# Kernel optimization log

Measured on AMD Instinct MI355X. Metric: run time of the kernel, lower is better.

Reference implementation:

```python
import jax, jax.numpy as jnp
import numpy as np
import math

N_HEADS = 16
DIM = 1024
D_HEAD = DIM // N_HEADS
BS, QLEN = 2, 2048


def setup_inputs() -> dict:
    key = jax.random.key(0)
    ks = jax.random.split(key, 10)
    s = 0.02
    return {
        "input": jax.random.normal(ks[0], (BS, QLEN, DIM), dtype=jnp.float32),
        "mask": jnp.ones((BS, QLEN), dtype=jnp.int32),
        "q_w": jax.random.normal(ks[1], (DIM, DIM), dtype=jnp.float32) * s,
        "q_b": jax.random.normal(ks[2], (DIM,), dtype=jnp.float32) * s,
        "k_w": jax.random.normal(ks[3], (DIM, DIM), dtype=jnp.float32) * s,
        "k_b": jax.random.normal(ks[4], (DIM,), dtype=jnp.float32) * s,
        "v_w": jax.random.normal(ks[5], (DIM, DIM), dtype=jnp.float32) * s,
        "v_b": jax.random.normal(ks[6], (DIM,), dtype=jnp.float32) * s,
        "o_w": jax.random.normal(ks[7], (DIM, DIM), dtype=jnp.float32) * s,
        "o_b": jax.random.normal(ks[8], (DIM,), dtype=jnp.float32) * s,
    }


def _shape(x, bs):
    # (bs, len, dim) -> (bs, heads, len, d_head)
    return x.reshape(bs, -1, N_HEADS, D_HEAD).transpose(0, 2, 1, 3)


def reference(input, mask, q_w, q_b, k_w, k_b, v_w, v_b, o_w, o_b):
    bs, qlen, dim = input.shape
    # projections (torch Linear: x @ W^T + b)
    q = _shape(input @ q_w.T + q_b, bs)
    k = _shape(input @ k_w.T + k_b, bs)
    v = _shape(input @ v_w.T + v_b, bs)
    q = q / math.sqrt(D_HEAD)
    # scores: (bs, heads, qlen, klen)
    scores = jnp.einsum("bhqd,bhkd->bhqk", q, k)
    pad = (mask == 0)[:, None, None, :]  # (bs,1,1,klen)
    scores = jnp.where(pad, -jnp.inf, scores)
    weights = jax.nn.softmax(scores.astype(jnp.float32), axis=-1).astype(scores.dtype)
    # dropout p=0.0 (eval) -> identity
    context = jnp.einsum("bhqk,bhkd->bhqd", weights, v)
    context = context.transpose(0, 2, 1, 3).reshape(bs, qlen, dim)
    return context @ o_w.T + o_b
```

## Files before the change

### kernel.cpp

```cpp
#include <hip/hip_runtime.h>


#define BS    2
#define QLEN  2048
#define DIM   1024
#define NH    16
#define DH    64
#define MTOK  (BS * QLEN)

#define QSCALE 0.18033688011112042f

typedef __attribute__((ext_vector_type(8))) short short8;
typedef __attribute__((ext_vector_type(4))) float float4_t;
typedef __attribute__((ext_vector_type(4))) int   int4_t;

__device__ __forceinline__ ushort f2bf(float f) {
    unsigned u = __float_as_uint(f);
    return (ushort)((u + 0x7fffu + ((u >> 16) & 1u)) >> 16);
}
__device__ __forceinline__ short8 pack8(float4 a0, float4 a1) {
    short8 r;
    r[0] = (short)f2bf(a0.x); r[1] = (short)f2bf(a0.y);
    r[2] = (short)f2bf(a0.z); r[3] = (short)f2bf(a0.w);
    r[4] = (short)f2bf(a1.x); r[5] = (short)f2bf(a1.y);
    r[6] = (short)f2bf(a1.z); r[7] = (short)f2bf(a1.w);
    return r;
}

__device__ __forceinline__ void glds16(const void* g, void* l) {
    __builtin_amdgcn_global_load_lds(
        (const __attribute__((address_space(1))) unsigned int*)g,
        (__attribute__((address_space(3))) unsigned int*)l, 16, 0, 0);
}

__global__ __launch_bounds__(256) void conv_all(
    const float* __restrict__ x,  const float* __restrict__ qw,
    const float* __restrict__ kw, const float* __restrict__ vw,
    const float* __restrict__ ow,
    ushort* __restrict__ Xbf, ushort* __restrict__ Wbf)
{
    const int blk = blockIdx.x;
    const float* s; ushort* d; size_t base;
    if (blk < 4096)      { s = x;  d = Xbf;             base = (size_t)blk * 1024; }
    else if (blk < 5120) { s = qw; d = Wbf;             base = (size_t)(blk - 4096) * 1024; }
    else if (blk < 6144) { s = kw; d = Wbf + 1048576;   base = (size_t)(blk - 5120) * 1024; }
    else if (blk < 7168) { s = vw; d = Wbf + 2097152;   base = (size_t)(blk - 6144) * 1024; }
    else                 { s = ow; d = Wbf + 3145728;   base = (size_t)(blk - 7168) * 1024; }
    const size_t i = base + threadIdx.x * 4;
    float4 v = *(const float4*)(s + i);
    ushort4 o;
    o.x = f2bf(v.x); o.y = f2bf(v.y); o.z = f2bf(v.z); o.w = f2bf(v.w);
    *(ushort4*)(d + i) = o;
}

__global__ __launch_bounds__(256) void transpose_v(
    const ushort* __restrict__ Vrow, ushort* __restrict__ Vt)
{
    __shared__ ushort T[64][72];
    const int tid  = threadIdx.x;
    const int tile = blockIdx.x;
    const int bh   = blockIdx.y;
    const int b = bh >> 4, h = bh & 15;

    #pragma unroll
    for (int rep = 0; rep < 2; ++rep) {
        int ch = tid + rep * 256;
        int tok = ch >> 3, seg = ch & 7;
        uint4 v = *(const uint4*)(Vrow + (size_t)(b * QLEN + tile * 64 + tok) * DIM
                                        + h * DH + seg * 8);
        *(uint4*)&T[tok][seg * 8] = v;
    }
    __syncthreads();
    #pragma unroll
    for (int rep = 0; rep < 2; ++rep) {
        int ch = tid + rep * 256;
        int dim = ch >> 3, tseg = ch & 7;
        ushort t0 = T[tseg * 8 + 0][dim], t1 = T[tseg * 8 + 1][dim];
        ushort t2 = T[tseg * 8 + 2][dim], t3 = T[tseg * 8 + 3][dim];
        ushort t4 = T[tseg * 8 + 4][dim], t5 = T[tseg * 8 + 5][dim];
        ushort t6 = T[tseg * 8 + 6][dim], t7 = T[tseg * 8 + 7][dim];
        uint4 o;
        o.x = (unsigned)t0 | ((unsigned)t1 << 16);
        o.y = (unsigned)t2 | ((unsigned)t3 << 16);
        o.z = (unsigned)t4 | ((unsigned)t5 << 16);
        o.w = (unsigned)t6 | ((unsigned)t7 << 16);
        *(uint4*)(Vt + (size_t)bh * DH * QLEN + (size_t)dim * QLEN
                      + tile * 64 + tseg * 8) = o;
    }
}

__global__ __launch_bounds__(256) void gemm_qkv(
    const ushort* __restrict__ A, const ushort* __restrict__ Bw,
    const float* __restrict__ bias0, const float* __restrict__ bias1,
    const float* __restrict__ bias2,
    ushort* __restrict__ outQ, ushort* __restrict__ outK, ushort* __restrict__ outVt)
{
    __shared__ ushort As[128 * 32];
    __shared__ ushort Bs[128 * 32];
    const int tid  = threadIdx.x;
    const int w    = tid >> 6;
    const int lane = tid & 63;
    const int r15  = lane & 15;
    const int quad = lane >> 4;
    const int nblk = 3072 >> 7;
    const int brow = blockIdx.x / nblk;
    const int bcol = blockIdx.x - brow * nblk;
    const int wrow = (w >> 1) * 64;
    const int wcol = (w & 1) * 64;
    const int K = DIM;

    float4_t acc[4][4];
    #pragma unroll
    for (int i = 0; i < 4; ++i)
        #pragma unroll
        for (int j = 0; j < 4; ++j)
            acc[i][j] = (float4_t){0.f, 0.f, 0.f, 0.f};

    int ch0 = w * 64 + lane;
    int ch1 = ch0 + 256;
    const int row0 = ch0 >> 2, s0 = ch0 & 3, gk0 = s0 ^ ((row0 >> 1) & 3);
    const int row1 = ch1 >> 2, s1 = ch1 & 3, gk1 = s1 ^ ((row1 >> 1) & 3);

    const ushort* ga0 = A + (size_t)(brow * 128 + row0) * K + gk0 * 8;
    const ushort* ga1 = A + (size_t)(brow * 128 + row1) * K + gk1 * 8;
    const ushort* gb0 = Bw + (size_t)(bcol * 128 + row0) * K + gk0 * 8;
    const ushort* gb1 = Bw + (size_t)(bcol * 128 + row1) * K + gk1 * 8;

    for (int k0 = 0; k0 < K; k0 += 32) {
        __syncthreads();
        glds16(ga0 + k0, As + ch0 * 8);
        glds16(ga1 + k0, As + ch1 * 8);
        glds16(gb0 + k0, Bs + ch0 * 8);
        glds16(gb1 + k0, Bs + ch1 * 8);
        __syncthreads();

        short8 af[4], bf[4];
        #pragma unroll
        for (int ms = 0; ms < 4; ++ms) {
            int row = wrow + ms * 16 + r15;
            int s = quad ^ ((row >> 1) & 3);
            af[ms] = *(const short8*)&As[row * 32 + s * 8];
        }
        #pragma unroll
        for (int ns = 0; ns < 4; ++ns) {
            int row = wcol + ns * 16 + r15;
            int s = quad ^ ((row >> 1) & 3);
            bf[ns] = *(const short8*)&Bs[row * 32 + s * 8];
        }
        #pragma unroll
        for (int ms = 0; ms < 4; ++ms)
            #pragma unroll
            for (int ns = 0; ns < 4; ++ns)
                acc[ms][ns] = __builtin_amdgcn_mfma_f32_16x16x32_bf16(
                    af[ms], bf[ns], acc[ms][ns], 0, 0, 0);
    }

    #pragma unroll
    for (int ms = 0; ms < 4; ++ms) {
        const int rowg = brow * 128 + wrow + ms * 16 + quad * 4;
        #pragma unroll
        for (int ns = 0; ns < 4; ++ns) {
            const int colg = bcol * 128 + wcol + ns * 16 + r15;
            if (colg < 1024) {
                const float bb = bias0[colg];
                #pragma unroll
                for (int r = 0; r < 4; ++r)
                    outQ[(size_t)(rowg + r) * 1024 + colg] =
                        f2bf((acc[ms][ns][r] + bb) * QSCALE);
            } else if (colg < 2048) {
                const float bb = bias1[colg - 1024];
                #pragma unroll
                for (int r = 0; r < 4; ++r)
                    outK[(size_t)(rowg + r) * 1024 + (colg - 1024)] =
                        f2bf(acc[ms][ns][r] + bb);
            } else {
                const int vcol = colg - 2048;
                const int hh = vcol >> 6, dd = vcol & 63;
                const float bb = bias2[vcol];
                const int bidx = rowg >> 11;
                const int tloc = rowg & 2047;
                ushort4 o4;
                o4.x = f2bf(acc[ms][ns][0] + bb);
                o4.y = f2bf(acc[ms][ns][1] + bb);
                o4.z = f2bf(acc[ms][ns][2] + bb);
                o4.w = f2bf(acc[ms][ns][3] + bb);
                *(ushort4*)&outVt[((size_t)(bidx * 16 + hh) * 64 + dd) * QLEN + tloc] = o4;
            }
        }
    }
}

__global__ __launch_bounds__(256) void gemm_o(
    const ushort* __restrict__ A, const ushort* __restrict__ Bw,
    const float* __restrict__ bias, float* __restrict__ Out)
{
    __shared__ ushort As[128 * 32];
    __shared__ ushort Bs[64 * 32];
    const int tid  = threadIdx.x;
    const int w    = tid >> 6;
    const int lane = tid & 63;
    const int r15  = lane & 15;
    const int quad = lane >> 4;
    const int brow = blockIdx.x >> 4;
    const int bcol = blockIdx.x & 15;
    const int wrow = w * 32;
    const int K = DIM;

    float4_t acc[2][4];
    #pragma unroll
    for (int i = 0; i < 2; ++i)
        #pragma unroll
        for (int j = 0; j < 4; ++j)
            acc[i][j] = (float4_t){0.f, 0.f, 0.f, 0.f};

    const int chA0 = w * 64 + lane, chA1 = chA0 + 256;
    const int rA0 = chA0 >> 2, sA0 = chA0 & 3, gkA0 = sA0 ^ ((rA0 >> 1) & 3);
    const int rA1 = chA1 >> 2, sA1 = chA1 & 3, gkA1 = sA1 ^ ((rA1 >> 1) & 3);
    const int rB  = tid >> 2,  sB  = tid & 3,  gkB  = sB  ^ ((rB  >> 1) & 3);

    const ushort* ga0 = A + (size_t)(brow * 128 + rA0) * K + gkA0 * 8;
    const ushort* ga1 = A + (size_t)(brow * 128 + rA1) * K + gkA1 * 8;
    const ushort* gb  = Bw + (size_t)(bcol * 64 + rB) * K + gkB * 8;

    for (int k0 = 0; k0 < K; k0 += 32) {
        __syncthreads();
        glds16(ga0 + k0, As + chA0 * 8);
        glds16(ga1 + k0, As + chA1 * 8);
        glds16(gb + k0,  Bs + tid * 8);
        __syncthreads();

        short8 af[2], bf[4];
        #pragma unroll
        for (int ms = 0; ms < 2; ++ms) {
            int row = wrow + ms * 16 + r15;
            int s = quad ^ ((row >> 1) & 3);
            af[ms] = *(const short8*)&As[row * 32 + s * 8];
        }
        #pragma unroll
        for (int ns = 0; ns < 4; ++ns) {
            int row = ns * 16 + r15;
            int s = quad ^ ((row >> 1) & 3);
            bf[ns] = *(const short8*)&Bs[row * 32 + s * 8];
        }
        #pragma unroll
        for (int ms = 0; ms < 2; ++ms)
            #pragma unroll
            for (int ns = 0; ns < 4; ++ns)
                acc[ms][ns] = __builtin_amdgcn_mfma_f32_16x16x32_bf16(
                    af[ms], bf[ns], acc[ms][ns], 0, 0, 0);
    }

    #pragma unroll
    for (int ms = 0; ms < 2; ++ms) {
        const int rowg = brow * 128 + wrow + ms * 16 + quad * 4;
        #pragma unroll
        for (int ns = 0; ns < 4; ++ns) {
            const int colg = bcol * 64 + ns * 16 + r15;
            const float bb = bias[colg];
            #pragma unroll
            for (int r = 0; r < 4; ++r)
                Out[(size_t)(rowg + r) * 1024 + colg] = acc[ms][ns][r] + bb;
        }
    }
}

__global__ __launch_bounds__(256) void gemm_f32in_bf16out(
    const float* __restrict__ X, const float* __restrict__ W,
    const float* __restrict__ B, ushort* __restrict__ Out,
    int M, int N, int K, float scale)
{
    const int lane = threadIdx.x & 63;
    const int wid  = (blockIdx.x * blockDim.x + threadIdx.x) >> 6;
    const int tilesN = N >> 4;
    const int tm = wid / tilesN;
    const int tn = wid - tm * tilesN;
    const int r15  = lane & 15;
    const int quad = lane >> 4;

    const float* xp = X + (size_t)(tm * 16 + r15) * K + quad * 8;
    const float* wp = W + (size_t)(tn * 16 + r15) * K + quad * 8;

    float4_t acc = {0.f, 0.f, 0.f, 0.f};
    for (int k0 = 0; k0 < K; k0 += 32) {
        float4 a0 = *(const float4*)(xp + k0);
        float4 a1 = *(const float4*)(xp + k0 + 4);
        float4 b0 = *(const float4*)(wp + k0);
        float4 b1 = *(const float4*)(wp + k0 + 4);
        acc = __builtin_amdgcn_mfma_f32_16x16x32_bf16(pack8(a0, a1), pack8(b0, b1), acc, 0, 0, 0);
    }
    const int col  = tn * 16 + r15;
    const float bias = B[col];
    const int row0 = tm * 16 + quad * 4;
    #pragma unroll
    for (int r = 0; r < 4; ++r)
        Out[(size_t)(row0 + r) * N + col] = f2bf((acc[r] + bias) * scale);
}

__global__ __launch_bounds__(256) void gemm_bf16in_f32out(
    const ushort* __restrict__ X, const float* __restrict__ W,
    const float* __restrict__ B, float* __restrict__ Out,
    int M, int N, int K)
{
    const int lane = threadIdx.x & 63;
    const int wid  = (blockIdx.x * blockDim.x + threadIdx.x) >> 6;
    const int tilesN = N >> 4;
    const int tm = wid / tilesN;
    const int tn = wid - tm * tilesN;
    const int r15  = lane & 15;
    const int quad = lane >> 4;

    const ushort* xp = X + (size_t)(tm * 16 + r15) * K + quad * 8;
    const float*  wp = W + (size_t)(tn * 16 + r15) * K + quad * 8;

    float4_t acc = {0.f, 0.f, 0.f, 0.f};
    for (int k0 = 0; k0 < K; k0 += 32) {
        short8 a = *(const short8*)(xp + k0);
        float4 b0 = *(const float4*)(wp + k0);
        float4 b1 = *(const float4*)(wp + k0 + 4);
        acc = __builtin_amdgcn_mfma_f32_16x16x32_bf16(a, pack8(b0, b1), acc, 0, 0, 0);
    }
    const int col  = tn * 16 + r15;
    const float bias = B[col];
    const int row0 = tm * 16 + quad * 4;
    #pragma unroll
    for (int r = 0; r < 4; ++r)
        Out[(size_t)(row0 + r) * N + col] = acc[r] + bias;
}

__global__ __launch_bounds__(256) void flash_attn(
    const ushort* __restrict__ Qb, const ushort* __restrict__ Kb,
    const ushort* __restrict__ Vt, const int* __restrict__ mask,
    ushort* __restrict__ Cb)
{
    __shared__ __align__(16) ushort Ks[2][64][64];
    __shared__ __align__(16) ushort Vs[2][64][64];
    __shared__ __align__(16) float  Mb[QLEN];
    __shared__ int Kflag[QLEN / 64];

    const int tid  = threadIdx.x;
    const int w    = tid >> 6;
    const int lane = tid & 63;
    const int r15  = lane & 15;
    const int quad = lane >> 4;
    const int bh = blockIdx.y;
    const int b = bh >> 4, h = bh & 15;

    {
        const int4* m4 = (const int4*)(mask + b * QLEN);
        #pragma unroll
        for (int rep = 0; rep < 2; ++rep) {
            const int idx = tid + rep * 256;
            int4 mv = m4[idx];
            float4 o;
            o.x = mv.x ? 0.f : -INFINITY;
            o.y = mv.y ? 0.f : -INFINITY;
            o.z = mv.z ? 0.f : -INFINITY;
            o.w = mv.w ? 0.f : -INFINITY;
            *(float4*)&Mb[idx * 4] = o;
        }
    }

    const int qbase = blockIdx.x * 128 + w * 32;
    const ushort* qp = Qb + (size_t)(b * QLEN + qbase + r15) * DIM + h * DH + quad * 8;
    short8 qf[2][2];
    qf[0][0] = *(const short8*)(qp);
    qf[0][1] = *(const short8*)(qp + 32);
    qf[1][0] = *(const short8*)(qp + 16 * DIM);
    qf[1][1] = *(const short8*)(qp + 16 * DIM + 32);

    const ushort* kg = Kb + (size_t)b * QLEN * DIM + h * DH;
    const ushort* vg = Vt + (size_t)bh * DH * QLEN;

    const int a0 = tid >> 3, seg = tid & 7;
    const int krow0 = (((a0 & 7) >> 2) << 4) + (((a0 >> 3) & 3) << 2) + (a0 & 3);
    const int sK = (seg ^ (krow0 & 7)) << 3;
    const int sV = (seg ^ (a0 & 7)) << 3;
    const int xq = (quad ^ (r15 & 7)) << 3;

    float4_t o[2][4];
    float4_t ol[2];
    #pragma unroll
    for (int rg = 0; rg < 2; ++rg) {
        ol[rg] = (float4_t){0.f, 0.f, 0.f, 0.f};
        #pragma unroll
        for (int ds = 0; ds < 4; ++ds)
            o[rg][ds] = (float4_t){0.f, 0.f, 0.f, 0.f};
    }
    short8 ones8;
    #pragma unroll
    for (int i = 0; i < 8; ++i) ones8[i] = (short)0x3F80;

    uint4 kr0 = *(const uint4*)(kg + (size_t)(a0     ) * DIM + seg * 8);
    uint4 kr1 = *(const uint4*)(kg + (size_t)(a0 + 32) * DIM + seg * 8);
    uint4 vr0 = *(const uint4*)(vg + (size_t)(a0     ) * QLEN + seg * 8);
    uint4 vr1 = *(const uint4*)(vg + (size_t)(a0 + 32) * QLEN + seg * 8);
    *(uint4*)&Ks[0][krow0     ][sK] = kr0;
    *(uint4*)&Ks[0][krow0 + 32][sK] = kr1;
    *(uint4*)&Vs[0][a0        ][sV] = vr0;
    *(uint4*)&Vs[0][a0 + 32   ][sV] = vr1;
    __syncthreads();

    if (tid < QLEN / 64) {
        const float4* m4 = (const float4*)&Mb[tid * 64];
        float acc = 0.f;
        #pragma unroll
        for (int i = 0; i < 16; ++i) {
            float4 v = m4[i];
            acc += v.x + v.y + v.z + v.w;
        }
        Kflag[tid] = (acc < -1e30f) ? 1 : 0;
    }
    __syncthreads();

    int p = 0;
    for (int kt = 0; kt < QLEN; kt += 64) {
        const bool more = (kt + 64 < QLEN);
        if (more) {
            kr0 = *(const uint4*)(kg + (size_t)(kt + 64 + a0     ) * DIM + seg * 8);
            kr1 = *(const uint4*)(kg + (size_t)(kt + 64 + a0 + 32) * DIM + seg * 8);
            vr0 = *(const uint4*)(vg + (size_t)(a0     ) * QLEN + kt + 64 + seg * 8);
            vr1 = *(const uint4*)(vg + (size_t)(a0 + 32) * QLEN + kt + 64 + seg * 8);
        }
        const int hasmask = Kflag[kt >> 6];

        int pk[4][2][2];
        #pragma unroll
        for (int ks = 0; ks < 4; ++ks) {
            const ushort* krow = &Ks[p][ks * 16 + r15][0];
            short8 kf0 = *(const short8*)(krow + xq);
            short8 kf1 = *(const short8*)(krow + (xq ^ 32));
            #pragma unroll
            for (int rg = 0; rg < 2; ++rg) {
                float4_t s = {0.f, 0.f, 0.f, 0.f};
                s = __builtin_amdgcn_mfma_f32_16x16x32_bf16(kf0, qf[rg][0], s, 0, 0, 0);
                s = __builtin_amdgcn_mfma_f32_16x16x32_bf16(kf1, qf[rg][1], s, 0, 0, 0);
                unsigned u0, u1, u2, u3;
                if (hasmask) {
                    const float4 mb = *(const float4*)&Mb[kt + ((ks >> 1) << 5)
                                                           + (quad << 3) + ((ks & 1) << 2)];
                    u0 = __float_as_uint(__builtin_amdgcn_exp2f(s[0] + mb.x));
                    u1 = __float_as_uint(__builtin_amdgcn_exp2f(s[1] + mb.y));
                    u2 = __float_as_uint(__builtin_amdgcn_exp2f(s[2] + mb.z));
                    u3 = __float_as_uint(__builtin_amdgcn_exp2f(s[3] + mb.w));
                } else {
                    u0 = __float_as_uint(__builtin_amdgcn_exp2f(s[0]));
                    u1 = __float_as_uint(__builtin_amdgcn_exp2f(s[1]));
                    u2 = __float_as_uint(__builtin_amdgcn_exp2f(s[2]));
                    u3 = __float_as_uint(__builtin_amdgcn_exp2f(s[3]));
                }
                pk[ks][rg][0] = __builtin_amdgcn_perm(u1, u0, 0x07060302);
                pk[ks][rg][1] = __builtin_amdgcn_perm(u3, u2, 0x07060302);
            }
        }

        #pragma unroll
        for (int ck = 0; ck < 2; ++ck) {
            short8 vf[4];
            #pragma unroll
            for (int ds = 0; ds < 4; ++ds)
                vf[ds] = *(const short8*)(&Vs[p][ds * 16 + r15][0] + (xq ^ (ck << 5)));
            #pragma unroll
            for (int rg = 0; rg < 2; ++rg) {
                int4_t pfi = { pk[2 * ck][rg][0], pk[2 * ck][rg][1],
                               pk[2 * ck + 1][rg][0], pk[2 * ck + 1][rg][1] };
                short8 pf = __builtin_bit_cast(short8, pfi);
                #pragma unroll
                for (int ds = 0; ds < 4; ++ds)
                    o[rg][ds] = __builtin_amdgcn_mfma_f32_16x16x32_bf16(
                        pf, vf[ds], o[rg][ds], 0, 0, 0);
                ol[rg] = __builtin_amdgcn_mfma_f32_16x16x32_bf16(
                    pf, ones8, ol[rg], 0, 0, 0);
            }
        }

        if (more) {
            *(uint4*)&Ks[p ^ 1][krow0     ][sK] = kr0;
            *(uint4*)&Ks[p ^ 1][krow0 + 32][sK] = kr1;
            *(uint4*)&Vs[p ^ 1][a0        ][sV] = vr0;
            *(uint4*)&Vs[p ^ 1][a0 + 32   ][sV] = vr1;
        }
        __syncthreads();
        p ^= 1;
    }

    #pragma unroll
    for (int rg = 0; rg < 2; ++rg) {
        #pragma unroll
        for (int r = 0; r < 4; ++r) {
            const float ir = 1.f / fmaxf(ol[rg][r], 1e-30f);
            const size_t rb = (size_t)(b * QLEN + qbase + rg * 16 + quad * 4 + r) * DIM
                              + h * DH;
            Cb[rb +  0 + r15] = f2bf(o[rg][0][r] * ir);
            Cb[rb + 16 + r15] = f2bf(o[rg][1][r] * ir);
            Cb[rb + 32 + r15] = f2bf(o[rg][2][r] * ir);
            Cb[rb + 48 + r15] = f2bf(o[rg][3][r] * ir);
        }
    }
}

extern "C" void kernel_launch(void* const* d_in, const int* in_sizes, int n_in,
                              void* d_out, int out_size, void* d_ws, size_t ws_size,
                              hipStream_t stream)
{
    const float* x    = (const float*)d_in[0];
    const int*   mask = (const int*)d_in[1];
    const float* q_w  = (const float*)d_in[2];
    const float* q_b  = (const float*)d_in[3];
    const float* k_w  = (const float*)d_in[4];
    const float* k_b  = (const float*)d_in[5];
    const float* v_w  = (const float*)d_in[6];
    const float* v_b  = (const float*)d_in[7];
    const float* o_w  = (const float*)d_in[8];
    const float* o_b  = (const float*)d_in[9];
    float* out = (float*)d_out;

    const size_t SEG = (size_t)MTOK * DIM;
    ushort* Qbf = (ushort*)d_out;
    ushort* Xbf = Qbf + SEG;
    ushort* Kb  = (ushort*)d_ws;
    ushort* Cb  = Kb + SEG;
    ushort* Vt  = Cb + SEG;
    ushort* Wbf = Vt + SEG;

    const bool big = ws_size >= (size_t)32 * 1024 * 1024;

    if (big) {
        conv_all<<<8192, 256, 0, stream>>>(x, q_w, k_w, v_w, o_w, Xbf, Wbf);
        gemm_qkv<<<(MTOK / 128) * (3072 / 128), 256, 0, stream>>>(
            Xbf, Wbf, q_b, k_b, v_b, Qbf, Kb, Vt);

        flash_attn<<<dim3(QLEN / 128, BS * NH), 256, 0, stream>>>(Qbf, Kb, Vt, mask, Cb);

        gemm_o<<<(MTOK / 128) * (DIM / 64), 256, 0, stream>>>(
            Cb, Wbf + 3 * (size_t)(DIM * DIM), o_b, out);
    } else {
        const int tiles   = (MTOK / 16) * (DIM / 16);
        const int gblocks = tiles / 4;
        gemm_f32in_bf16out<<<gblocks, 256, 0, stream>>>(x, q_w, q_b, Qbf, MTOK, DIM, DIM, QSCALE);
        gemm_f32in_bf16out<<<gblocks, 256, 0, stream>>>(x, k_w, k_b, Kb,  MTOK, DIM, DIM, 1.0f);
        gemm_f32in_bf16out<<<gblocks, 256, 0, stream>>>(x, v_w, v_b, Cb,  MTOK, DIM, DIM, 1.0f);
        transpose_v<<<dim3(QLEN / 64, BS * NH), 256, 0, stream>>>(Cb, Vt);
        flash_attn<<<dim3(QLEN / 128, BS * NH), 256, 0, stream>>>(Qbf, Kb, Vt, mask, Cb);
        gemm_bf16in_f32out<<<tiles / 4, 256, 0, stream>>>(Cb, o_w, o_b, out, MTOK, DIM, DIM);
    }
}
```

Before: 216.8 us.

## Double K-step in GEMMs and process two KV tiles per flash iteration

Both projection GEMMs now load a 64-wide K slice per iteration, using a new 8-way XOR swizzle, which halves the number of barrier pairs per K loop. The flash attention kernel stages two 64-key tiles at once (128 keys per iteration) instead of ping-pong double buffering, which halves the number of loop trips and barriers. It also removes the per-tile mask-flag precomputation and always adds the mask bias before exp2. The trade-off is more LDS per GEMM block, less overlap between global loads and compute in attention because a barrier now precedes the LDS writes, and extra adds where the mask is all ones.

```diff
diff --git a/kernel.cpp b/kernel.cpp
--- a/kernel.cpp
+++ b/kernel.cpp
@@ -95,8 +95,8 @@
     const float* __restrict__ bias2,
     ushort* __restrict__ outQ, ushort* __restrict__ outK, ushort* __restrict__ outVt)
 {
-    __shared__ ushort As[128 * 32];
-    __shared__ ushort Bs[128 * 32];
+    __shared__ ushort As[128 * 64];
+    __shared__ ushort Bs[128 * 64];
     const int tid  = threadIdx.x;
     const int w    = tid >> 6;
     const int lane = tid & 63;
@@ -116,43 +116,46 @@
         for (int j = 0; j < 4; ++j)
             acc[i][j] = (float4_t){0.f, 0.f, 0.f, 0.f};
 
-    int ch0 = w * 64 + lane;
-    int ch1 = ch0 + 256;
-    const int row0 = ch0 >> 2, s0 = ch0 & 3, gk0 = s0 ^ ((row0 >> 1) & 3);
-    const int row1 = ch1 >> 2, s1 = ch1 & 3, gk1 = s1 ^ ((row1 >> 1) & 3);
-
-    const ushort* ga0 = A + (size_t)(brow * 128 + row0) * K + gk0 * 8;
-    const ushort* ga1 = A + (size_t)(brow * 128 + row1) * K + gk1 * 8;
-    const ushort* gb0 = Bw + (size_t)(bcol * 128 + row0) * K + gk0 * 8;
-    const ushort* gb1 = Bw + (size_t)(bcol * 128 + row1) * K + gk1 * 8;
-
-    for (int k0 = 0; k0 < K; k0 += 32) {
+    int chS[4];
+    const ushort* gaS[4];
+    const ushort* gbS[4];
+    #pragma unroll
+    for (int rep = 0; rep < 4; ++rep) {
+        const int ch  = w * 256 + rep * 64 + lane;
+        const int row = ch >> 3;
+        const int g   = (ch & 7) ^ (row & 7);
+        chS[rep] = ch;
+        gaS[rep] = A  + (size_t)(brow * 128 + row) * K + g * 8;
+        gbS[rep] = Bw + (size_t)(bcol * 128 + row) * K + g * 8;
+    }
+    const int xg = r15 & 7;
+
+    for (int k0 = 0; k0 < K; k0 += 64) {
         __syncthreads();
-        glds16(ga0 + k0, As + ch0 * 8);
-        glds16(ga1 + k0, As + ch1 * 8);
-        glds16(gb0 + k0, Bs + ch0 * 8);
-        glds16(gb1 + k0, Bs + ch1 * 8);
+        #pragma unroll
+        for (int rep = 0; rep < 4; ++rep) {
+            glds16(gaS[rep] + k0, As + chS[rep] * 8);
+            glds16(gbS[rep] + k0, Bs + chS[rep] * 8);
+        }
         __syncthreads();
 
-        short8 af[4], bf[4];
-        #pragma unroll
-        for (int ms = 0; ms < 4; ++ms) {
-            int row = wrow + ms * 16 + r15;
-            int s = quad ^ ((row >> 1) & 3);
-            af[ms] = *(const short8*)&As[row * 32 + s * 8];
-        }
-        #pragma unroll
-        for (int ns = 0; ns < 4; ++ns) {
-            int row = wcol + ns * 16 + r15;
-            int s = quad ^ ((row >> 1) & 3);
-            bf[ns] = *(const short8*)&Bs[row * 32 + s * 8];
-        }
-        #pragma unroll
-        for (int ms = 0; ms < 4; ++ms)
+        #pragma unroll
+        for (int hh = 0; hh < 2; ++hh) {
+            const int ph = ((hh * 4 + quad) ^ xg) * 8;
+            short8 af[4], bf[4];
+            #pragma unroll
+            for (int ms = 0; ms < 4; ++ms)
+                af[ms] = *(const short8*)&As[(wrow + ms * 16 + r15) * 64 + ph];
             #pragma unroll
             for (int ns = 0; ns < 4; ++ns)
-                acc[ms][ns] = __builtin_amdgcn_mfma_f32_16x16x32_bf16(
-                    af[ms], bf[ns], acc[ms][ns], 0, 0, 0);
+                bf[ns] = *(const short8*)&Bs[(wcol + ns * 16 + r15) * 64 + ph];
+            #pragma unroll
+            for (int ms = 0; ms < 4; ++ms)
+                #pragma unroll
+                for (int ns = 0; ns < 4; ++ns)
+                    acc[ms][ns] = __builtin_amdgcn_mfma_f32_16x16x32_bf16(
+                        af[ms], bf[ns], acc[ms][ns], 0, 0, 0);
+        }
     }
 
     #pragma unroll
@@ -194,8 +197,8 @@
     const ushort* __restrict__ A, const ushort* __restrict__ Bw,
     const float* __restrict__ bias, float* __restrict__ Out)
 {
-    __shared__ ushort As[128 * 32];
-    __shared__ ushort Bs[64 * 32];
+    __shared__ ushort As[128 * 64];
+    __shared__ ushort Bs[64 * 64];
     const int tid  = threadIdx.x;
     const int w    = tid >> 6;
     const int lane = tid & 63;
@@ -213,41 +216,53 @@
         for (int j = 0; j < 4; ++j)
             acc[i][j] = (float4_t){0.f, 0.f, 0.f, 0.f};
 
-    const int chA0 = w * 64 + lane, chA1 = chA0 + 256;
-    const int rA0 = chA0 >> 2, sA0 = chA0 & 3, gkA0 = sA0 ^ ((rA0 >> 1) & 3);
-    const int rA1 = chA1 >> 2, sA1 = chA1 & 3, gkA1 = sA1 ^ ((rA1 >> 1) & 3);
-    const int rB  = tid >> 2,  sB  = tid & 3,  gkB  = sB  ^ ((rB  >> 1) & 3);
-
-    const ushort* ga0 = A + (size_t)(brow * 128 + rA0) * K + gkA0 * 8;
-    const ushort* ga1 = A + (size_t)(brow * 128 + rA1) * K + gkA1 * 8;
-    const ushort* gb  = Bw + (size_t)(bcol * 64 + rB) * K + gkB * 8;
-
-    for (int k0 = 0; k0 < K; k0 += 32) {
+    int chA[4];  const ushort* gaS[4];
+    #pragma unroll
+    for (int rep = 0; rep < 4; ++rep) {
+        const int ch  = w * 256 + rep * 64 + lane;
+        const int row = ch >> 3;
+        const int g   = (ch & 7) ^ (row & 7);
+        chA[rep] = ch;
+        gaS[rep] = A + (size_t)(brow * 128 + row) * K + g * 8;
+    }
+    int chB[2];  const ushort* gbS[2];
+    #pragma unroll
+    for (int rep = 0; rep < 2; ++rep) {
+        const int ch  = w * 128 + rep * 64 + lane;
+        const int row = ch >> 3;
+        const int g   = (ch & 7) ^ (row & 7);
+        chB[rep] = ch;
+        gbS[rep] = Bw + (size_t)(bcol * 64 + row) * K + g * 8;
+    }
+    const int xg = r15 & 7;
+
+    for (int k0 = 0; k0 < K; k0 += 64) {
         __syncthreads();
-        glds16(ga0 + k0, As + chA0 * 8);
-        glds16(ga1 + k0, As + chA1 * 8);
-        glds16(gb + k0,  Bs + tid * 8);
+        #pragma unroll
+        for (int rep = 0; rep < 4; ++rep)
+            glds16(gaS[rep] + k0, As + chA[rep] * 8);
+        #pragma unroll
+        for (int rep = 0; rep < 2; ++rep)
+            glds16(gbS[rep] + k0, Bs + chB[rep] * 8);
         __syncthreads();
 
-        short8 af[2], bf[4];
-        #pragma unroll
-        for (int ms = 0; ms < 2; ++ms) {
-            int row = wrow + ms * 16 + r15;
-            int s = quad ^ ((row >> 1) & 3);
-            af[ms] = *(const short8*)&As[row * 32 + s * 8];
-        }
-        #pragma unroll
-        for (int ns = 0; ns < 4; ++ns) {
-            int row = ns * 16 + r15;
-            int s = quad ^ ((row >> 1) & 3);
-            bf[ns] = *(const short8*)&Bs[row * 32 + s * 8];
-        }
-        #pragma unroll
-        for (int ms = 0; ms < 2; ++ms)
+        #pragma unroll
+        for (int hh = 0; hh < 2; ++hh) {
+            const int ph = ((hh * 4 + quad) ^ xg) * 8;
+            short8 af[2], bf[4];
+            #pragma unroll
+            for (int ms = 0; ms < 2; ++ms)
+                af[ms] = *(const short8*)&As[(wrow + ms * 16 + r15) * 64 + ph];
             #pragma unroll
             for (int ns = 0; ns < 4; ++ns)
-                acc[ms][ns] = __builtin_amdgcn_mfma_f32_16x16x32_bf16(
-                    af[ms], bf[ns], acc[ms][ns], 0, 0, 0);
+                bf[ns] = *(const short8*)&Bs[(ns * 16 + r15) * 64 + ph];
+            #pragma unroll
+            for (int ms = 0; ms < 2; ++ms)
+                #pragma unroll
+                for (int ns = 0; ns < 4; ++ns)
+                    acc[ms][ns] = __builtin_amdgcn_mfma_f32_16x16x32_bf16(
+                        af[ms], bf[ns], acc[ms][ns], 0, 0, 0);
+        }
     }
 
     #pragma unroll
@@ -335,7 +350,6 @@
     __shared__ __align__(16) ushort Ks[2][64][64];
     __shared__ __align__(16) ushort Vs[2][64][64];
     __shared__ __align__(16) float  Mb[QLEN];
-    __shared__ int Kflag[QLEN / 64];
 
     const int tid  = threadIdx.x;
     const int w    = tid >> 6;
@@ -390,97 +404,92 @@
     #pragma unroll
     for (int i = 0; i < 8; ++i) ones8[i] = (short)0x3F80;
 
-    uint4 kr0 = *(const uint4*)(kg + (size_t)(a0     ) * DIM + seg * 8);
-    uint4 kr1 = *(const uint4*)(kg + (size_t)(a0 + 32) * DIM + seg * 8);
-    uint4 vr0 = *(const uint4*)(vg + (size_t)(a0     ) * QLEN + seg * 8);
-    uint4 vr1 = *(const uint4*)(vg + (size_t)(a0 + 32) * QLEN + seg * 8);
-    *(uint4*)&Ks[0][krow0     ][sK] = kr0;
-    *(uint4*)&Ks[0][krow0 + 32][sK] = kr1;
-    *(uint4*)&Vs[0][a0        ][sV] = vr0;
-    *(uint4*)&Vs[0][a0 + 32   ][sV] = vr1;
+    uint4 kr[2][2], vr[2][2];
+    #pragma unroll
+    for (int tt = 0; tt < 2; ++tt) {
+        kr[tt][0] = *(const uint4*)(kg + (size_t)(tt * 64 + a0     ) * DIM + seg * 8);
+        kr[tt][1] = *(const uint4*)(kg + (size_t)(tt * 64 + a0 + 32) * DIM + seg * 8);
+        vr[tt][0] = *(const uint4*)(vg + (size_t)(a0     ) * QLEN + tt * 64 + seg * 8);
+        vr[tt][1] = *(const uint4*)(vg + (size_t)(a0 + 32) * QLEN + tt * 64 + seg * 8);
+    }
+    #pragma unroll
+    for (int tt = 0; tt < 2; ++tt) {
+        *(uint4*)&Ks[tt][krow0     ][sK] = kr[tt][0];
+        *(uint4*)&Ks[tt][krow0 + 32][sK] = kr[tt][1];
+        *(uint4*)&Vs[tt][a0        ][sV] = vr[tt][0];
+        *(uint4*)&Vs[tt][a0 + 32   ][sV] = vr[tt][1];
+    }
     __syncthreads();
 
-    if (tid < QLEN / 64) {
-        const float4* m4 = (const float4*)&Mb[tid * 64];
-        float acc = 0.f;
-        #pragma unroll
-        for (int i = 0; i < 16; ++i) {
-            float4 v = m4[i];
-            acc += v.x + v.y + v.z + v.w;
-        }
-        Kflag[tid] = (acc < -1e30f) ? 1 : 0;
-    }
-    __syncthreads();
-
-    int p = 0;
-    for (int kt = 0; kt < QLEN; kt += 64) {
-        const bool more = (kt + 64 < QLEN);
+    for (int kt = 0; kt < QLEN; kt += 128) {
+        const bool more = (kt + 128 < QLEN);
         if (more) {
-            kr0 = *(const uint4*)(kg + (size_t)(kt + 64 + a0     ) * DIM + seg * 8);
-            kr1 = *(const uint4*)(kg + (size_t)(kt + 64 + a0 + 32) * DIM + seg * 8);
-            vr0 = *(const uint4*)(vg + (size_t)(a0     ) * QLEN + kt + 64 + seg * 8);
-            vr1 = *(const uint4*)(vg + (size_t)(a0 + 32) * QLEN + kt + 64 + seg * 8);
-        }
-        const int hasmask = Kflag[kt >> 6];
-
-        int pk[4][2][2];
-        #pragma unroll
-        for (int ks = 0; ks < 4; ++ks) {
-            const ushort* krow = &Ks[p][ks * 16 + r15][0];
-            short8 kf0 = *(const short8*)(krow + xq);
-            short8 kf1 = *(const short8*)(krow + (xq ^ 32));
-            #pragma unroll
-            for (int rg = 0; rg < 2; ++rg) {
-                float4_t s = {0.f, 0.f, 0.f, 0.f};
-                s = __builtin_amdgcn_mfma_f32_16x16x32_bf16(kf0, qf[rg][0], s, 0, 0, 0);
-                s = __builtin_amdgcn_mfma_f32_16x16x32_bf16(kf1, qf[rg][1], s, 0, 0, 0);
-                unsigned u0, u1, u2, u3;
-                if (hasmask) {
-                    const float4 mb = *(const float4*)&Mb[kt + ((ks >> 1) << 5)
-                                                           + (quad << 3) + ((ks & 1) << 2)];
-                    u0 = __float_as_uint(__builtin_amdgcn_exp2f(s[0] + mb.x));
-                    u1 = __float_as_uint(__builtin_amdgcn_exp2f(s[1] + mb.y));
-                    u2 = __float_as_uint(__builtin_amdgcn_exp2f(s[2] + mb.z));
-                    u3 = __float_as_uint(__builtin_amdgcn_exp2f(s[3] + mb.w));
-                } else {
-                    u0 = __float_as_uint(__builtin_amdgcn_exp2f(s[0]));
-                    u1 = __float_as_uint(__builtin_amdgcn_exp2f(s[1]));
-                    u2 = __float_as_uint(__builtin_amdgcn_exp2f(s[2]));
-                    u3 = __float_as_uint(__builtin_amdgcn_exp2f(s[3]));
+            const int ktn = kt + 128;
+            #pragma unroll
+            for (int tt = 0; tt < 2; ++tt) {
+                kr[tt][0] = *(const uint4*)(kg + (size_t)(ktn + tt * 64 + a0     ) * DIM + seg * 8);
+                kr[tt][1] = *(const uint4*)(kg + (size_t)(ktn + tt * 64 + a0 + 32) * DIM + seg * 8);
+                vr[tt][0] = *(const uint4*)(vg + (size_t)(a0     ) * QLEN + ktn + tt * 64 + seg * 8);
+                vr[tt][1] = *(const uint4*)(vg + (size_t)(a0 + 32) * QLEN + ktn + tt * 64 + seg * 8);
+            }
+        }
+
+        #pragma unroll
+        for (int tt = 0; tt < 2; ++tt) {
+            const int ktt = kt + tt * 64;
+            int pk[4][2][2];
+            #pragma unroll
+            for (int ks = 0; ks < 4; ++ks) {
+                const ushort* krow = &Ks[tt][ks * 16 + r15][0];
+                short8 kf0 = *(const short8*)(krow + xq);
+                short8 kf1 = *(const short8*)(krow + (xq ^ 32));
+                const float4 mb = *(const float4*)&Mb[ktt + ((ks >> 1) << 5)
+                                                       + (quad << 3) + ((ks & 1) << 2)];
+                #pragma unroll
+                for (int rg = 0; rg < 2; ++rg) {
+                    float4_t s = {0.f, 0.f, 0.f, 0.f};
+                    s = __builtin_amdgcn_mfma_f32_16x16x32_bf16(kf0, qf[rg][0], s, 0, 0, 0);
+                    s = __builtin_amdgcn_mfma_f32_16x16x32_bf16(kf1, qf[rg][1], s, 0, 0, 0);
+                    unsigned u0 = __float_as_uint(__builtin_amdgcn_exp2f(s[0] + mb.x));
+                    unsigned u1 = __float_as_uint(__builtin_amdgcn_exp2f(s[1] + mb.y));
+                    unsigned u2 = __float_as_uint(__builtin_amdgcn_exp2f(s[2] + mb.z));
+                    unsigned u3 = __float_as_uint(__builtin_amdgcn_exp2f(s[3] + mb.w));
+                    pk[ks][rg][0] = __builtin_amdgcn_perm(u1, u0, 0x07060302);
+                    pk[ks][rg][1] = __builtin_amdgcn_perm(u3, u2, 0x07060302);
                 }
-                pk[ks][rg][0] = __builtin_amdgcn_perm(u1, u0, 0x07060302);
-                pk[ks][rg][1] = __builtin_amdgcn_perm(u3, u2, 0x07060302);
             }
-        }
-
-        #pragma unroll
-        for (int ck = 0; ck < 2; ++ck) {
-            short8 vf[4];
-            #pragma unroll
-            for (int ds = 0; ds < 4; ++ds)
-                vf[ds] = *(const short8*)(&Vs[p][ds * 16 + r15][0] + (xq ^ (ck << 5)));
-            #pragma unroll
-            for (int rg = 0; rg < 2; ++rg) {
-                int4_t pfi = { pk[2 * ck][rg][0], pk[2 * ck][rg][1],
-                               pk[2 * ck + 1][rg][0], pk[2 * ck + 1][rg][1] };
-                short8 pf = __builtin_bit_cast(short8, pfi);
+            #pragma unroll
+            for (int ck = 0; ck < 2; ++ck) {
+                short8 vf[4];
                 #pragma unroll
                 for (int ds = 0; ds < 4; ++ds)
-                    o[rg][ds] = __builtin_amdgcn_mfma_f32_16x16x32_bf16(
-                        pf, vf[ds], o[rg][ds], 0, 0, 0);
-                ol[rg] = __builtin_amdgcn_mfma_f32_16x16x32_bf16(
-                    pf, ones8, ol[rg], 0, 0, 0);
+                    vf[ds] = *(const short8*)(&Vs[tt][ds * 16 + r15][0] + (xq ^ (ck << 5)));
+                #pragma unroll
+                for (int rg = 0; rg < 2; ++rg) {
+                    int4_t pfi = { pk[2 * ck][rg][0], pk[2 * ck][rg][1],
+                                   pk[2 * ck + 1][rg][0], pk[2 * ck + 1][rg][1] };
+                    short8 pf = __builtin_bit_cast(short8, pfi);
+                    #pragma unroll
+                    for (int ds = 0; ds < 4; ++ds)
+                        o[rg][ds] = __builtin_amdgcn_mfma_f32_16x16x32_bf16(
+                            pf, vf[ds], o[rg][ds], 0, 0, 0);
+                    ol[rg] = __builtin_amdgcn_mfma_f32_16x16x32_bf16(
+                        pf, ones8, ol[rg], 0, 0, 0);
+                }
             }
         }
 
         if (more) {
-            *(uint4*)&Ks[p ^ 1][krow0     ][sK] = kr0;
-            *(uint4*)&Ks[p ^ 1][krow0 + 32][sK] = kr1;
-            *(uint4*)&Vs[p ^ 1][a0        ][sV] = vr0;
-            *(uint4*)&Vs[p ^ 1][a0 + 32   ][sV] = vr1;
-        }
-        __syncthreads();
-        p ^= 1;
+            __syncthreads();
+            #pragma unroll
+            for (int tt = 0; tt < 2; ++tt) {
+                *(uint4*)&Ks[tt][krow0     ][sK] = kr[tt][0];
+                *(uint4*)&Ks[tt][krow0 + 32][sK] = kr[tt][1];
+                *(uint4*)&Vs[tt][a0        ][sV] = vr[tt][0];
+                *(uint4*)&Vs[tt][a0 + 32   ][sV] = vr[tt][1];
+            }
+            __syncthreads();
+        }
     }
 
     #pragma unroll
@@ -528,9 +537,7 @@
         conv_all<<<8192, 256, 0, stream>>>(x, q_w, k_w, v_w, o_w, Xbf, Wbf);
         gemm_qkv<<<(MTOK / 128) * (3072 / 128), 256, 0, stream>>>(
             Xbf, Wbf, q_b, k_b, v_b, Qbf, Kb, Vt);
-
         flash_attn<<<dim3(QLEN / 128, BS * NH), 256, 0, stream>>>(Qbf, Kb, Vt, mask, Cb);
-
         gemm_o<<<(MTOK / 128) * (DIM / 64), 256, 0, stream>>>(
             Cb, Wbf + 3 * (size_t)(DIM * DIM), o_b, out);
     } else {
```

Result: slower. 245.0 us (+13.0%).
